# Optimization experiments

Measured on AMD Instinct MI355X. Metric: run time of the kernel, lower is better.

Reference implementation:

```python
import jax, jax.numpy as jnp
from jax import lax
import numpy as np


def setup_inputs() -> dict:
    key = jax.random.key(0)
    k1, k2, k3, k4 = jax.random.split(key, 4)
    B, L, T = 8192, 48, 49  # batch of sentence pairs, len_A, extended_length_B+1
    emissions = jax.random.normal(k1, (B, L, T), dtype=jnp.float32)
    trans_feats = jax.random.normal(k2, (T, T, 6), dtype=jnp.float32)
    w2 = jax.random.normal(k3, (6,), dtype=jnp.float32)
    b2 = jax.random.normal(k4, (1,), dtype=jnp.float32)
    return {"emissions": emissions, "trans_feats": trans_feats, "w2": w2, "b2": b2}


def reference(emissions, trans_feats, w2, b2):
    """Batched CRF forward algorithm (_forward_alg with max_span_size=1).

    emissions:   [B, len_A, T]  word-pair interaction scores (output_both)
    trans_feats: [T, T, 6]      6-dim transition features; mlp2 maps -> scalar
    Returns alpha (log partition) per batch element, shape [B].
    """
    B, L, T = emissions.shape
    # mlp2: Linear(6, 1). trans[j, k] = score of transitioning from state k to j.
    trans = jnp.einsum('jkf,f->jk', trans_feats, w2) + b2[0]
    # Original indexes feat[j-1]: state j uses emission column (j-1) mod T.
    emit = jnp.roll(emissions, 1, axis=2)  # [B, L, T]
    # i == 0: forward_var starts at 0, no transition; logsumexp over the
    # broadcast emit score adds log(T).
    f0 = emit[:, 0, :] + jnp.log(jnp.asarray(T, dtype=emissions.dtype))  # [B, T]

    def step(f, e_i):
        # f: [B, T] previous forward vars; next[b, j] = lse_k(f[b,k] + trans[j,k]) + e_i[b,j]
        nf = jax.nn.logsumexp(f[:, None, :] + trans[None, :, :], axis=2) + e_i
        return nf, None

    fL, _ = lax.scan(step, f0, jnp.moveaxis(emit[:, 1:, :], 1, 0))  # scan over len_A-1 steps
    alpha = jax.nn.logsumexp(fL, axis=1)  # [B]
    return alpha
```

## Files before the change

kernel.cpp:

```cpp
#include <hip/hip_runtime.h>
#include <math.h>

#define TS 49
#define LOG49 3.8918202981106265f
#define LN2 0.6931471805599453f

typedef short bf16x8 __attribute__((ext_vector_type(8)));
typedef float f32x4 __attribute__((ext_vector_type(4)));
typedef float f32x4u __attribute__((ext_vector_type(4), aligned(4)));


__global__ void prep_kernel(const float* __restrict__ tf, const float* __restrict__ w2,
                            const float* __restrict__ b2, float* __restrict__ ws) {
    __shared__ float tr[TS * TS];
    __shared__ float red[256];
    const int tid = threadIdx.x;
    const float w0 = w2[0], w1 = w2[1], w2v = w2[2], w3 = w2[3], w4 = w2[4], w5 = w2[5];
    const float bb = b2[0];
    float lmax = -INFINITY;
    for (int idx = tid; idx < TS * TS; idx += 256) {
        const float* p = tf + idx * 6;
        float s = bb + p[0]*w0 + p[1]*w1 + p[2]*w2v + p[3]*w3 + p[4]*w4 + p[5]*w5;
        tr[idx] = s;
        lmax = fmaxf(lmax, s);
    }
    red[tid] = lmax;
    __syncthreads();
    for (int s = 128; s > 0; s >>= 1) {
        if (tid < s) red[tid] = fmaxf(red[tid], red[tid + s]);
        __syncthreads();
    }
    const float Tmax = red[0];
    __syncthreads();
    unsigned short* B = (unsigned short*)ws;
    for (int idx = tid; idx < 4096; idx += 256) {
        const int s  = idx & 7;
        const int l  = (idx >> 3) & 63;
        const int h  = (idx >> 9) & 1;
        const int nt = idx >> 10;
        const int jp = 4 * (l & 15) + nt;
        const int kp = 32 * h + 8 * (l >> 4) + s;
        float v = 0.0f;
        if (jp < TS && kp < TS) {
            const int jj = (jp + 1) % TS, kk = (kp + 1) % TS;
            v = __expf(tr[jj * TS + kk] - Tmax);
        }
        unsigned bts = __float_as_uint(v);
        B[idx] = (unsigned short)((bts + 0x7FFFu + ((bts >> 16) & 1u)) >> 16);
    }
    if (tid == 0) ((float*)ws)[2048] = Tmax;
}

__device__ __forceinline__ unsigned cvtpk_bf16(float lo, float hi) {
    unsigned d;
    asm("v_cvt_pk_bf16_f32 %0, %1, %2" : "=v"(d) : "v"(lo), "v"(hi));
    return d;
}

__global__ __launch_bounds__(64, 2) void crf_fwd(const float* __restrict__ emis,
                                                 const unsigned short* __restrict__ wsB,
                                                 float* __restrict__ out, int L) {
    __shared__ __align__(16) unsigned short V16[1024];
    const int l = threadIdx.x, g = l >> 4, c0 = l & 15;
    const int b0 = blockIdx.x * 8;
    const float Tmax = ((const float*)wsB)[2048];

    bf16x8 Bf[4][2];
    {
        const bf16x8* Bt = (const bf16x8*)wsB;
        #pragma unroll
        for (int nt = 0; nt < 4; ++nt)
            #pragma unroll
            for (int h = 0; h < 2; ++h) Bf[nt][h] = Bt[(nt * 2 + h) * 64 + l];
    }

    int wi[4];
    #pragma unroll
    for (int t = 0; t < 4; ++t) {
        const int ch = 4 * g + t;
        wi[t] = ch * 16 + (c0 ^ ((ch & 7) << 1));
    }
    const int ra0 = c0 * 8 + (g ^ (c0 & 7));
    const int ra1 = c0 * 8 + ((4 + g) ^ (c0 & 7));
    uint2* const Vw = (uint2*)V16;
    const bf16x8* const Vr = (const bf16x8*)V16;

    {
        const uint2 z = {0u, 0u};
        Vw[wi[2]] = z;
        Vw[wi[3]] = z;
    }

    const int LT = L * TS;
    const bool sel12 = (c0 >= 12);
    const int col4 = sel12 ? 45 : 4 * c0;
    const float* ebase[2];
    #pragma unroll
    for (int t = 0; t < 2; ++t)
        ebase[t] = emis + (size_t)(b0 + 2 * g + t) * LT + col4;

    f32x4 pf[4][2];

#define LQ(STEP, SLOT) do {                                                           \
    _Pragma("unroll")                                                                 \
    for (int t = 0; t < 2; ++t)                                                       \
        pf[SLOT][t] = *(const f32x4u*)(ebase[t] + (STEP) * TS);                       \
} while (0)

#define EESEL(DST, SLOT) do {                                                         \
    _Pragma("unroll")                                                                 \
    for (int t = 0; t < 2; ++t) {                                                     \
        const f32x4 q = pf[SLOT][t];                                                  \
        DST[0][t] = __expf(sel12 ? q.w : q.x);                                        \
        DST[1][t] = __expf(q.y);                                                      \
        DST[2][t] = __expf(q.z);                                                      \
        DST[3][t] = __expf(q.w);                                                      \
    }                                                                                 \
} while (0)

    LQ(0, 0);
    if (L > 1) LQ(1, 1);
    if (L > 2) LQ(2, 2);
    if (L > 3) LQ(3, 3);

    float v[4][2];
    #pragma unroll
    for (int t = 0; t < 2; ++t) {
        const f32x4 q = pf[0][t];
        const float i0 = sel12 ? q.w : q.x;
        v[0][t] = (4 * c0 + 0 < TS) ? __expf(i0)  : 0.0f;
        v[1][t] = (4 * c0 + 1 < TS) ? __expf(q.y) : 0.0f;
        v[2][t] = (4 * c0 + 2 < TS) ? __expf(q.z) : 0.0f;
        v[3][t] = (4 * c0 + 3 < TS) ? __expf(q.w) : 0.0f;
    }

    float ee0[4][2], ee1[4][2];
    EESEL(ee1, 1);

    float sc[2]   = {0.f, 0.f};
    float fac[2]  = {1.f, 1.f};
    float pend[2] = {0.f, 0.f};

#define STEP(I, EC, EN, SN, SL, DO_C, DO_A) do {                                      \
                  \
    _Pragma("unroll")                                                                 \
    for (int t = 0; t < 2; ++t) {                                                     \
        uint2 u;                                                                      \
        u.x = cvtpk_bf16(v[0][t], v[1][t]);                                           \
        u.y = cvtpk_bf16(v[2][t], v[3][t]);                                           \
        Vw[wi[t]] = u;                                                                \
    }                                                                                 \
                   \
    EESEL(EN, SN);                                                                    \
                                 \
    if ((I) + 3 < L) LQ((I) + 3, SL);                                                 \
    asm volatile("" ::: "memory");                                                    \
                      \
    const bf16x8 A0 = Vr[ra0];                                                        \
    const bf16x8 A1 = Vr[ra1];                                                        \
                          \
    _Pragma("unroll")                                                                 \
    for (int nt = 0; nt < 4; ++nt) {                                                  \
        f32x4 acc = {0.f, 0.f, 0.f, 0.f};                                             \
        acc = __builtin_amdgcn_mfma_f32_16x16x32_bf16(A0, Bf[nt][0], acc, 0, 0, 0);   \
        acc = __builtin_amdgcn_mfma_f32_16x16x32_bf16(A1, Bf[nt][1], acc, 0, 0, 0);   \
        _Pragma("unroll")                                                             \
        for (int t = 0; t < 2; ++t) {                                                 \
            float nv = acc[t] * EC[nt][t];                                            \
            if (DO_A) nv *= fac[t];                                                   \
            v[nt][t] = nv;                                                            \
        }                                                                             \
    }                                                                                 \
    if (DO_A) {                                                                       \
        _Pragma("unroll")                                                             \
        for (int t = 0; t < 2; ++t) sc[t] += pend[t];                                 \
    }                                                                                 \
                         \
    if (DO_C) {                                                                       \
        _Pragma("unroll")                                                             \
        for (int t = 0; t < 2; ++t) {                                                 \
            float mx = fmaxf(fmaxf(v[0][t], v[1][t]), fmaxf(v[2][t], v[3][t]));       \
            mx = fmaxf(mx, __shfl_xor(mx, 1, 64));                                    \
            mx = fmaxf(mx, __shfl_xor(mx, 2, 64));                                    \
            mx = fmaxf(mx, __shfl_xor(mx, 4, 64));                                    \
            mx = fmaxf(mx, __shfl_xor(mx, 8, 64));                                    \
            const unsigned ex = __float_as_uint(mx) >> 23;                            \
            fac[t]  = __uint_as_float((254u - ex) << 23);                             \
            pend[t] = (float)((int)ex - 127) * LN2;                                   \
        }                                                                             \
    }                                                                                 \
} while (0)

    const int S = L - 1;
    int i = 1;
    for (; i + 3 <= S; i += 4) {
        STEP(i + 0, ee1, ee0, 2, 0, 1, 0);
        STEP(i + 1, ee0, ee1, 3, 1, 0, 1);
        STEP(i + 2, ee1, ee0, 0, 2, 0, 0);
        STEP(i + 3, ee0, ee1, 1, 3, 0, 0);
    }
    if (i <= S)     STEP(i,     ee1, ee0, 2, 0, 1, 0);
    if (i + 1 <= S) STEP(i + 1, ee0, ee1, 3, 1, 0, 1);
    if (i + 2 <= S) STEP(i + 2, ee1, ee0, 0, 2, 0, 0);
#undef STEP
#undef EESEL
#undef LQ

    float res[2];
    #pragma unroll
    for (int t = 0; t < 2; ++t) {
        float s = (v[0][t] + v[1][t]) + (v[2][t] + v[3][t]);
        s += __shfl_xor(s, 1, 64);
        s += __shfl_xor(s, 2, 64);
        s += __shfl_xor(s, 4, 64);
        s += __shfl_xor(s, 8, 64);
        res[t] = sc[t] + __logf(s) + LOG49 + (float)(L - 1) * Tmax;
    }
    if (c0 == 0) {
        #pragma unroll
        for (int t = 0; t < 2; ++t) out[b0 + 2 * g + t] = res[t];
    }
}

extern "C" void kernel_launch(void* const* d_in, const int* in_sizes, int n_in,
                              void* d_out, int out_size, void* d_ws, size_t ws_size,
                              hipStream_t stream) {
    const float* emis = (const float*)d_in[0];
    const float* tf   = (const float*)d_in[1];
    const float* w2   = (const float*)d_in[2];
    const float* b2   = (const float*)d_in[3];
    float* out = (float*)d_out;
    float* ws  = (float*)d_ws;

    const int B = out_size;
    const int L = in_sizes[0] / (B * TS);

    prep_kernel<<<1, 256, 0, stream>>>(tf, w2, b2, ws);
    crf_fwd<<<B / 8, 64, 0, stream>>>(emis, (const unsigned short*)ws, out, L);
}
```

Before: 29.21 us.

## Process four batch rows per wave instead of eight to double block count

Each 64-thread block now handles 4 batch elements (one per 16-lane group) instead of 8, so the grid grows from B/8 to B/4 blocks. The serial per-step chain per wave is shorter because each lane handles one row instead of two, and there are more waves to hide latency. In exchange, the MFMA's 16 rows are only a quarter used (more zero-padded rows), so total matrix and LDS work per batch element roughly doubles.

```diff
diff --git a/kernel.cpp b/kernel.cpp
--- a/kernel.cpp
+++ b/kernel.cpp
@@ -62,7 +62,7 @@
                                                  float* __restrict__ out, int L) {
     __shared__ __align__(16) unsigned short V16[1024];
     const int l = threadIdx.x, g = l >> 4, c0 = l & 15;
-    const int b0 = blockIdx.x * 8;
+    const int b0 = blockIdx.x * 4;
     const float Tmax = ((const float*)wsB)[2048];
 
     bf16x8 Bf[4][2];
@@ -87,6 +87,7 @@
 
     {
         const uint2 z = {0u, 0u};
+        Vw[wi[1]] = z;
         Vw[wi[2]] = z;
         Vw[wi[3]] = z;
     }
@@ -94,28 +95,20 @@
     const int LT = L * TS;
     const bool sel12 = (c0 >= 12);
     const int col4 = sel12 ? 45 : 4 * c0;
-    const float* ebase[2];
-    #pragma unroll
-    for (int t = 0; t < 2; ++t)
-        ebase[t] = emis + (size_t)(b0 + 2 * g + t) * LT + col4;
-
-    f32x4 pf[4][2];
+    const float* const ebase = emis + (size_t)(b0 + g) * LT + col4;
+
+    f32x4 pf[4];
 
 #define LQ(STEP, SLOT) do {                                                           \
-    _Pragma("unroll")                                                                 \
-    for (int t = 0; t < 2; ++t)                                                       \
-        pf[SLOT][t] = *(const f32x4u*)(ebase[t] + (STEP) * TS);                       \
+    pf[SLOT] = *(const f32x4u*)(ebase + (STEP) * TS);                                 \
 } while (0)
 
 #define EESEL(DST, SLOT) do {                                                         \
-    _Pragma("unroll")                                                                 \
-    for (int t = 0; t < 2; ++t) {                                                     \
-        const f32x4 q = pf[SLOT][t];                                                  \
-        DST[0][t] = __expf(sel12 ? q.w : q.x);                                        \
-        DST[1][t] = __expf(q.y);                                                      \
-        DST[2][t] = __expf(q.z);                                                      \
-        DST[3][t] = __expf(q.w);                                                      \
-    }                                                                                 \
+    const f32x4 q = pf[SLOT];                                                         \
+    DST[0] = __expf(sel12 ? q.w : q.x);                                               \
+    DST[1] = __expf(q.y);                                                             \
+    DST[2] = __expf(q.z);                                                             \
+    DST[3] = __expf(q.w);                                                             \
 } while (0)
 
     LQ(0, 0);
@@ -123,32 +116,28 @@
     if (L > 2) LQ(2, 2);
     if (L > 3) LQ(3, 3);
 
-    float v[4][2];
-    #pragma unroll
-    for (int t = 0; t < 2; ++t) {
-        const f32x4 q = pf[0][t];
+    float v[4];
+    {
+        const f32x4 q = pf[0];
         const float i0 = sel12 ? q.w : q.x;
-        v[0][t] = (4 * c0 + 0 < TS) ? __expf(i0)  : 0.0f;
-        v[1][t] = (4 * c0 + 1 < TS) ? __expf(q.y) : 0.0f;
-        v[2][t] = (4 * c0 + 2 < TS) ? __expf(q.z) : 0.0f;
-        v[3][t] = (4 * c0 + 3 < TS) ? __expf(q.w) : 0.0f;
-    }
-
-    float ee0[4][2], ee1[4][2];
+        v[0] = (4 * c0 + 0 < TS) ? __expf(i0)  : 0.0f;
+        v[1] = (4 * c0 + 1 < TS) ? __expf(q.y) : 0.0f;
+        v[2] = (4 * c0 + 2 < TS) ? __expf(q.z) : 0.0f;
+        v[3] = (4 * c0 + 3 < TS) ? __expf(q.w) : 0.0f;
+    }
+
+    float ee0[4], ee1[4];
     EESEL(ee1, 1);
 
-    float sc[2]   = {0.f, 0.f};
-    float fac[2]  = {1.f, 1.f};
-    float pend[2] = {0.f, 0.f};
+    float sc = 0.f, fac = 1.f, pend = 0.f;
 
 #define STEP(I, EC, EN, SN, SL, DO_C, DO_A) do {                                      \
-                  \
-    _Pragma("unroll")                                                                 \
-    for (int t = 0; t < 2; ++t) {                                                     \
+                          \
+    {                                                                                 \
         uint2 u;                                                                      \
-        u.x = cvtpk_bf16(v[0][t], v[1][t]);                                           \
-        u.y = cvtpk_bf16(v[2][t], v[3][t]);                                           \
-        Vw[wi[t]] = u;                                                                \
+        u.x = cvtpk_bf16(v[0], v[1]);                                                 \
+        u.y = cvtpk_bf16(v[2], v[3]);                                                 \
+        Vw[wi[0]] = u;                                                                \
     }                                                                                 \
                    \
     EESEL(EN, SN);                                                                    \
@@ -158,36 +147,27 @@
                       \
     const bf16x8 A0 = Vr[ra0];                                                        \
     const bf16x8 A1 = Vr[ra1];                                                        \
-                          \
+                           \
     _Pragma("unroll")                                                                 \
     for (int nt = 0; nt < 4; ++nt) {                                                  \
         f32x4 acc = {0.f, 0.f, 0.f, 0.f};                                             \
         acc = __builtin_amdgcn_mfma_f32_16x16x32_bf16(A0, Bf[nt][0], acc, 0, 0, 0);   \
         acc = __builtin_amdgcn_mfma_f32_16x16x32_bf16(A1, Bf[nt][1], acc, 0, 0, 0);   \
-        _Pragma("unroll")                                                             \
-        for (int t = 0; t < 2; ++t) {                                                 \
-            float nv = acc[t] * EC[nt][t];                                            \
-            if (DO_A) nv *= fac[t];                                                   \
-            v[nt][t] = nv;                                                            \
-        }                                                                             \
+        float nv = acc[0] * EC[nt];                                                   \
+        if (DO_A) nv *= fac;                                                          \
+        v[nt] = nv;                                                                   \
     }                                                                                 \
-    if (DO_A) {                                                                       \
-        _Pragma("unroll")                                                             \
-        for (int t = 0; t < 2; ++t) sc[t] += pend[t];                                 \
-    }                                                                                 \
+    if (DO_A) sc += pend;                                                             \
                          \
     if (DO_C) {                                                                       \
-        _Pragma("unroll")                                                             \
-        for (int t = 0; t < 2; ++t) {                                                 \
-            float mx = fmaxf(fmaxf(v[0][t], v[1][t]), fmaxf(v[2][t], v[3][t]));       \
-            mx = fmaxf(mx, __shfl_xor(mx, 1, 64));                                    \
-            mx = fmaxf(mx, __shfl_xor(mx, 2, 64));                                    \
-            mx = fmaxf(mx, __shfl_xor(mx, 4, 64));                                    \
-            mx = fmaxf(mx, __shfl_xor(mx, 8, 64));                                    \
-            const unsigned ex = __float_as_uint(mx) >> 23;                            \
-            fac[t]  = __uint_as_float((254u - ex) << 23);                             \
-            pend[t] = (float)((int)ex - 127) * LN2;                                   \
-        }                                                                             \
+        float mx = fmaxf(fmaxf(v[0], v[1]), fmaxf(v[2], v[3]));                       \
+        mx = fmaxf(mx, __shfl_xor(mx, 1, 64));                                        \
+        mx = fmaxf(mx, __shfl_xor(mx, 2, 64));                                        \
+        mx = fmaxf(mx, __shfl_xor(mx, 4, 64));                                        \
+        mx = fmaxf(mx, __shfl_xor(mx, 8, 64));                                        \
+        const unsigned ex = __float_as_uint(mx) >> 23;                                \
+        fac  = __uint_as_float((254u - ex) << 23);                                    \
+        pend = (float)((int)ex - 127) * LN2;                                          \
     }                                                                                 \
 } while (0)
 
@@ -206,20 +186,13 @@
 #undef EESEL
 #undef LQ
 
-    float res[2];
-    #pragma unroll
-    for (int t = 0; t < 2; ++t) {
-        float s = (v[0][t] + v[1][t]) + (v[2][t] + v[3][t]);
-        s += __shfl_xor(s, 1, 64);
-        s += __shfl_xor(s, 2, 64);
-        s += __shfl_xor(s, 4, 64);
-        s += __shfl_xor(s, 8, 64);
-        res[t] = sc[t] + __logf(s) + LOG49 + (float)(L - 1) * Tmax;
-    }
-    if (c0 == 0) {
-        #pragma unroll
-        for (int t = 0; t < 2; ++t) out[b0 + 2 * g + t] = res[t];
-    }
+    float s = (v[0] + v[1]) + (v[2] + v[3]);
+    s += __shfl_xor(s, 1, 64);
+    s += __shfl_xor(s, 2, 64);
+    s += __shfl_xor(s, 4, 64);
+    s += __shfl_xor(s, 8, 64);
+    const float res = sc + __logf(s) + LOG49 + (float)(L - 1) * Tmax;
+    if (c0 == 0) out[b0 + g] = res;
 }
 
 extern "C" void kernel_launch(void* const* d_in, const int* in_sizes, int n_in,
@@ -236,5 +209,5 @@
     const int L = in_sizes[0] / (B * TS);
 
     prep_kernel<<<1, 256, 0, stream>>>(tf, w2, b2, ws);
-    crf_fwd<<<B / 8, 64, 0, stream>>>(emis, (const unsigned short*)ws, out, L);
-}
+    crf_fwd<<<B / 4, 64, 0, stream>>>(emis, (const unsigned short*)ws, out, L);
+}
```

Measured after the change: 28.60 us. -2.1%, faster.
